# Kernel optimization log

Hardware: AMD Instinct MI355X
Metric: run time of the kernel (lower is better)

## Reference

```python
import jax, jax.numpy as jnp
import numpy as np

B, C1, C2, N1, N2 = 8, 16, 32, 256, 128


def _masks():
    # static numpy masks, mirroring EquivariantLayer.__init__
    n_max, n_min = max(N1, N2), min(N1, N2)
    k = np.arange(n_max)
    k[k > n_max // 2] -= n_max
    mask = np.abs(k) <= n_min / 2            # |k| <= n_min/2 (both nyquists)
    mask2 = mask[: n_max // 2 + 1].copy()    # taken BEFORE removing neg nyquist
    nyq_pos = k == n_min / 2
    nyq_pos2 = nyq_pos[: n_max // 2 + 1]
    nyq_neg = k == -n_min / 2
    mask[nyq_neg] = False                    # drop negative nyquist row
    return mask, mask2, nyq_pos, nyq_pos2

MASK, MASK2, NYQ_POS, NYQ_POS2 = _masks()


def rot90_kernel(t):
    # 90-deg rotation about grid point [0,0] for periodic kernels:
    # transpose last two dims, keep column 0, reverse remaining columns
    t = jnp.swapaxes(t, -1, -2)
    return jnp.concatenate([t[..., :1], t[..., 1:][..., ::-1]], axis=-1)


def symmetric_kernel(kernel):
    # average over the 8 elements of D4 (rotations + transpose*rotations)
    k1 = kernel
    k2 = rot90_kernel(k1)
    k3 = rot90_kernel(k2)
    k4 = rot90_kernel(k3)
    k5 = jnp.swapaxes(k1, -1, -2)
    k6 = rot90_kernel(k5)
    k7 = rot90_kernel(k6)
    k8 = rot90_kernel(k7)
    return (k1 + k2 + k3 + k4 + k5 + k6 + k7 + k8) / 8.0


def _forward(f, kernel):
    F = jnp.fft.rfft2(f)                                  # [b,c1,N1,N1//2+1]
    # downsample: zero nyquist modes, truncate spectrum, rescale
    F = jnp.where(jnp.asarray(NYQ_POS)[None, None, :, None], 0, F)
    F = jnp.where(jnp.asarray(NYQ_POS2)[None, None, None, :], 0, F)
    F = F[:, :, MASK, :][:, :, :, MASK2] * (N2 / N1) ** 2  # [b,c1,N2,N2//2+1]
    # spectral convolution with D4-symmetrized kernel
    K = jnp.fft.rfft2(symmetric_kernel(kernel))            # [1,c1,c2,N2,N2//2+1]
    conv = jnp.einsum('bcnk,cdnk->bdnk', F, K[0])          # sum over input channels
    return jnp.fft.irfft2(F), jnp.fft.irfft2(conv)


def setup_inputs() -> dict:
    key = jax.random.key(0)
    kf, kk = jax.random.split(key)
    f = jax.random.normal(kf, (B, C1, N1, N1), dtype=jnp.float32)
    eps = 0.1
    kernel = eps * (2.0 * jax.random.uniform(kk, (1, C1, C2, N2, N2), dtype=jnp.float32) - 1.0)
    return {"f": f, "kernel": kernel}


def reference(f, kernel):
    return _forward(f, kernel)
```

## Files before the change

kernel.cpp:

```cpp
#include <hip/hip_runtime.h>

#define PI_F 3.14159265358979f

__device__ __forceinline__ float2 cmul(float2 a, float2 b) {
    return make_float2(a.x * b.x - a.y * b.y, a.x * b.y + a.y * b.x);
}
__device__ __forceinline__ float2 cadd(float2 a, float2 b) { return make_float2(a.x + b.x, a.y + b.y); }
__device__ __forceinline__ float2 csub(float2 a, float2 b) { return make_float2(a.x - b.x, a.y - b.y); }
__device__ __forceinline__ float2 shflx(float2 v, int m) {
    return make_float2(__shfl_xor(v.x, m, 64), __shfl_xor(v.y, m, 64));
}
__device__ __forceinline__ float2 shfli(float2 v, int src) {
    return make_float2(__shfl(v.x, src, 64), __shfl(v.y, src, 64));
}
__device__ __forceinline__ int brev6(int x) { return (int)(__brev((unsigned)x) >> 26); }

template<int CTRL>
__device__ __forceinline__ float dpp1(float x) {
    return __builtin_bit_cast(float, __builtin_amdgcn_update_dpp(
        0, __builtin_bit_cast(int, x), CTRL, 0xF, 0xF, true));
}
template<int CTRL>
__device__ __forceinline__ float2 dppx(float2 v) {
    return make_float2(dpp1<CTRL>(v.x), dpp1<CTRL>(v.y));
}
template<int M>
__device__ __forceinline__ float2 xorx(float2 v) {
    if constexpr (M == 1)      return dppx<0xB1>(v);
    else if constexpr (M == 2) return dppx<0x4E>(v);
    else if constexpr (M == 8) return dppx<0x128>(v);
    else                       return shflx(v, M);
}

template<bool INV>
__device__ __forceinline__ void tw_init(int lane, float2* w, float* sg) {
#pragma unroll
    for (int t = 0; t < 6; ++t) {
        int m = 32 >> t;
        bool up = (lane & m) != 0;
        int pos = lane & (m - 1);
        float ang = (INV ? PI_F : -PI_F) * (float)pos / (float)m;
        float sn, cs;
        __sincosf(ang, &sn, &cs);
        w[t]  = up ? make_float2(cs, sn) : make_float2(1.f, 0.f);
        sg[t] = up ? -1.f : 1.f;
    }
}

__device__ __forceinline__ float2 fft64s(float2 v, const float2* w, const float* sg) {
#define FFT_STAGE(T, M) { float2 p = xorx<M>(v);                                   \
        float2 d = make_float2(fmaf(sg[T], v.x, p.x), fmaf(sg[T], v.y, p.y));      \
        v = cmul(d, w[T]); }
    FFT_STAGE(0, 32) FFT_STAGE(1, 16) FFT_STAGE(2, 8)
    FFT_STAGE(3, 4)  FFT_STAGE(4, 2)  FFT_STAGE(5, 1)
#undef FFT_STAGE
    return v;
}

__device__ void kfft_body(const float* __restrict__ kin, float* __restrict__ kout,
                          float2* X, int img) {
    int lane = threadIdx.x & 63, wv = threadIdx.x >> 6;
    float2 w[6]; float sg[6];
    tw_init<false>(lane, w, sg);
    int b6 = brev6(lane);
    float sn, cs;
    __sincosf(-PI_F * (float)lane * (1.0f / 64.0f), &sn, &cs);
    float2 w64 = make_float2(cs, sn);
    __sincosf(-PI_F * (float)b6 * (1.0f / 64.0f), &sn, &cs);
    float2 wub = make_float2(cs, sn);
    const float2* in2 = (const float2*)(kin + (size_t)img * 16384);
    int gm2 = brev6((64 - b6) & 63);
#pragma unroll 2
    for (int rr = 0; rr < 16; ++rr) {
        int r = wv * 16 + rr;
        float2 z = in2[r * 64 + lane];
        z = fft64s(z, w, sg);
        float2 zm = shfli(z, gm2);
        float ar = z.x + zm.x, ai = z.y - zm.y;
        float br = z.x - zm.x, bi = z.y + zm.y;
        float p = wub.x * br - wub.y * bi, q = wub.x * bi + wub.y * br;
        X[r * 65 + b6] = make_float2(0.5f * (ar + q), 0.5f * (ai - p));
    }
    __syncthreads();
    float2 c0[8], c1[8];
#pragma unroll
    for (int cc = 0; cc < 8; ++cc) {
        int k = wv * 8 + cc;
        c0[cc] = X[lane * 65 + k];
        c1[cc] = X[(lane + 64) * 65 + k];
    }
    __syncthreads();
    float* Rr = (float*)X;
#pragma unroll
    for (int cc = 0; cc < 8; ++cc) {
        int k = wv * 8 + cc;
        float2 r0 = c0[cc], r1 = c1[cc];
        float2 t = r0;
        r0 = cadd(t, r1);
        r1 = cmul(csub(t, r1), w64);
        r0 = fft64s(r0, w, sg);
        r1 = fft64s(r1, w, sg);
        Rr[(2 * b6) * 65 + k]     = r0.x;
        Rr[(2 * b6 + 1) * 65 + k] = r1.x;
    }
    __syncthreads();
    float4* ko4 = (float4*)(kout + (size_t)img * 8192);
    for (int i = threadIdx.x; i < 2048; i += 512) {
        int n = i >> 4, k4 = (i & 15) << 2;
        float4 o;
        float* op = (float*)&o;
#pragma unroll
        for (int m = 0; m < 4; ++m) {
            int k = k4 + m;
            float t1 = Rr[n * 65 + k];
            float t2 = Rr[((128 - n) & 127) * 65 + k];
            float t3, t4;
            if (n < 64) {
                t3 = Rr[k * 65 + n];
                t4 = Rr[((128 - k) & 127) * 65 + n];
            } else {
                int c2 = 128 - n; if (c2 > 63) c2 = 63;
                t3 = Rr[((128 - k) & 127) * 65 + c2];
                t4 = Rr[k * 65 + c2];
            }
            op[m] = 0.25f * (t1 + t2 + t3 + t4);
        }
        ko4[i] = o;
    }
}

__device__ void fcol_body(const float2* __restrict__ G, float2* __restrict__ FH,
                          float2* S, int bid) {
    int img = bid >> 2, q = bid & 3;
    int lane = threadIdx.x & 63, wv = threadIdx.x >> 6;
    float2 w[6]; float sg[6];
    tw_init<false>(lane, w, sg);
    float sn, cs;
    __sincosf(-PI_F * (float)lane * (1.0f / 64.0f), &sn, &cs);
    float2 w64 = make_float2(cs, sn);
    __sincosf(-PI_F * (float)lane * (1.0f / 128.0f), &sn, &cs);
    float2 w128a = make_float2(cs, sn);
    __sincosf(-PI_F * (float)(lane + 64) * (1.0f / 128.0f), &sn, &cs);
    float2 w128b = make_float2(cs, sn);
    const float2* src = G + (size_t)img * 16384 + q * 16;
    for (int i = threadIdx.x; i < 4096; i += 512) {
        int r = i >> 4, c = i & 15;
        S[r * 17 + c] = src[(size_t)r * 64 + c];
    }
    __syncthreads();
    float2 q0[2], q1[2], q2[2], q3[2];
#pragma unroll
    for (int cc = 0; cc < 2; ++cc) {
        int c = wv * 2 + cc;
        q0[cc] = S[(lane)       * 17 + c];
        q1[cc] = S[(lane +  64) * 17 + c];
        q2[cc] = S[(lane + 128) * 17 + c];
        q3[cc] = S[(lane + 192) * 17 + c];
    }
    __syncthreads();
    int b6 = brev6(lane);
#pragma unroll
    for (int cc = 0; cc < 2; ++cc) {
        int c = wv * 2 + cc;
        float2 r0 = q0[cc], r1 = q1[cc], r2 = q2[cc], r3 = q3[cc], t;
        t = r0; r0 = cadd(t, r2); r2 = cmul(csub(t, r2), w128a);
        t = r1; r1 = cadd(t, r3); r3 = cmul(csub(t, r3), w128b);
        t = r0; r0 = cadd(t, r1); r1 = cmul(csub(t, r1), w64);
        t = r2; r2 = cadd(t, r3); r3 = cmul(csub(t, r3), w64);
        r0 = fft64s(r0, w, sg); r1 = fft64s(r1, w, sg);
        r2 = fft64s(r2, w, sg); r3 = fft64s(r3, w, sg);
        float2 vv[4] = { r0, r2, r1, r3 };
#pragma unroll
        for (int j = 0; j < 4; ++j) {
            int n = 4 * b6 + j;
            int r = (n < 64) ? n : ((n >= 193) ? n - 128 : -1);
            if (r >= 0) S[r * 17 + c] = make_float2(vv[j].x * 0.25f, vv[j].y * 0.25f);
        }
    }
    __syncthreads();
    float2* dst = FH + (size_t)img * 8192 + q * 16;
    for (int i = threadIdx.x; i < 2048; i += 512) {
        int r = i >> 4, c = i & 15;
        float2 v = (r == 64) ? make_float2(0.f, 0.f) : S[r * 17 + c];
        dst[(size_t)r * 64 + c] = v;
    }
}

__device__ void einsum_body(const float2* __restrict__ F, const float* __restrict__ K,
                            float2* __restrict__ C, float2* Ft, int bid) {
    int nk0 = bid * 32;
    int t = threadIdx.x;
    for (int i = t; i < 4096; i += 512) {
        int bc = i >> 5, nl = i & 31;
        Ft[i] = F[(size_t)bc * 8192 + nk0 + nl];
    }
    __syncthreads();
    int nl = t & 31, dg = t >> 5;
    int nk = nk0 + nl;
    float2 acc[2][8] = {};
#pragma unroll
    for (int c = 0; c < 16; ++c) {
        float2 fv[8];
#pragma unroll
        for (int b = 0; b < 8; ++b) fv[b] = Ft[(b * 16 + c) * 32 + nl];
#pragma unroll
        for (int j = 0; j < 2; ++j) {
            int d = j * 16 + dg;
            float kv = K[(size_t)(c * 32 + d) * 8192 + nk];
#pragma unroll
            for (int b = 0; b < 8; ++b) {
                acc[j][b].x = fmaf(fv[b].x, kv, acc[j][b].x);
                acc[j][b].y = fmaf(fv[b].y, kv, acc[j][b].y);
            }
        }
    }
#pragma unroll
    for (int j = 0; j < 2; ++j) {
        int d = j * 16 + dg;
#pragma unroll
        for (int b = 0; b < 8; ++b)
            C[(size_t)(b * 32 + d) * 8192 + nk] = acc[j][b];
    }
}

__device__ void ifuse_body(const float2* __restrict__ src, float2* __restrict__ dst,
                           float2* S) {
    int lane = threadIdx.x & 63, wv = threadIdx.x >> 6;
    float2 w[6]; float sg[6];
    tw_init<true>(lane, w, sg);
    float sn, cs;
    __sincosf(PI_F * (float)lane * (1.0f / 64.0f), &sn, &cs);
    float2 w64 = make_float2(cs, sn);
    for (int i = threadIdx.x; i < 8192; i += 512) {
        int r = i >> 6, c = i & 63;
        S[r * 65 + c] = src[i];
    }
    __syncthreads();
    float2 c0[8], c1[8];
#pragma unroll
    for (int cc = 0; cc < 8; ++cc) {
        int k = wv * 8 + cc;
        c0[cc] = S[lane * 65 + k];
        c1[cc] = S[(lane + 64) * 65 + k];
    }
    __syncthreads();
    int b6 = brev6(lane);
#pragma unroll
    for (int cc = 0; cc < 8; ++cc) {
        int k = wv * 8 + cc;
        float2 r0 = c0[cc], r1 = c1[cc];
        float2 t = r0;
        r0 = cadd(t, r1);
        r1 = cmul(csub(t, r1), w64);
        r0 = fft64s(r0, w, sg);
        r1 = fft64s(r1, w, sg);
        S[(2 * b6) * 65 + k]     = r0;
        S[(2 * b6 + 1) * 65 + k] = r1;
    }
    __syncthreads();
#pragma unroll 2
    for (int rr = 0; rr < 16; ++rr) {
        int m = wv * 16 + rr;
        float2 X = S[m * 65 + lane];
        float2 Xm = shfli(X, (64 - lane) & 63);
        if (lane == 0) Xm = make_float2(0.f, 0.f);
        float er = 0.5f * (X.x + Xm.x), ei = 0.5f * (X.y - Xm.y);
        float br = 0.5f * (X.x - Xm.x), bi = 0.5f * (X.y + Xm.y);
        float orr = w64.x * br - w64.y * bi, oi = w64.x * bi + w64.y * br;
        float2 Z = make_float2(er - oi, ei + orr);
        Z = fft64s(Z, w, sg);
        Z = shfli(Z, b6);
        dst[m * 64 + lane] = make_float2(Z.x * (1.0f / 8192.0f), Z.y * (1.0f / 8192.0f));
    }
}

__global__ __launch_bounds__(256) void rfft256(const float* __restrict__ f,
                                               float2* __restrict__ G) {
    int lane = threadIdx.x & 63, wv = threadIdx.x >> 6;
    int row0 = (blockIdx.x * 4 + wv) * 8;
    float2 w[6]; float sg[6];
    tw_init<false>(lane, w, sg);
    float sn, cs;
    __sincosf(-PI_F * (float)lane * (1.0f / 64.0f), &sn, &cs);
    float2 w64 = make_float2(cs, sn);
    __sincosf(-PI_F * (float)lane * (1.0f / 128.0f), &sn, &cs);
    float2 wu = make_float2(cs, sn);
    int srcK = brev6(lane >> 1);
    int srcM = brev6((64 - ((lane + 1) >> 1)) & 63);
#pragma unroll 2
    for (int rr = 0; rr < 8; ++rr) {
        size_t row = (size_t)(row0 + rr);
        const float2* x = (const float2*)(f + row * 256);
        float2 r0 = x[lane], r1 = x[lane + 64];
        float2 t = r0;
        r0 = cadd(t, r1);
        r1 = cmul(csub(t, r1), w64);
        r0 = fft64s(r0, w, sg);
        r1 = fft64s(r1, w, sg);
        float2 e0 = shfli(r0, srcK), o0 = shfli(r1, srcK);
        float2 zk = (lane & 1) ? o0 : e0;
        float2 e1 = shfli(r0, srcM), o1 = shfli(r1, srcM);
        float2 zm = (lane & 1) ? o1 : e1;
        float ar = zk.x + zm.x, ai = zk.y - zm.y;
        float br = zk.x - zm.x, bi = zk.y + zm.y;
        float p = wu.x * br - wu.y * bi, q = wu.x * bi + wu.y * br;
        G[row * 64 + lane] = make_float2(0.5f * (ar + q), 0.5f * (ai - p));
    }
}

__global__ __launch_bounds__(512) void mega1(const float* __restrict__ kin,
                                             float* __restrict__ Kr,
                                             const float2* __restrict__ G,
                                             float2* __restrict__ FH) {
    __shared__ float2 SH[128 * 65];
    int bid = blockIdx.x;
    if (bid < 512) kfft_body(kin, Kr, SH, bid);
    else           fcol_body(G, FH, SH, bid - 512);
}

__global__ __launch_bounds__(512) void mega2(const float2* __restrict__ FH,
                                             const float* __restrict__ Kr,
                                             float2* __restrict__ CONV,
                                             float* __restrict__ out) {
    __shared__ float2 SH[128 * 65];
    int bid = blockIdx.x;
    if (bid < 256) einsum_body(FH, Kr, CONV, SH, bid);
    else {
        int img = bid - 256;
        ifuse_body(FH + (size_t)img * 8192, (float2*)(out + (size_t)img * 16384), SH);
    }
}

__global__ __launch_bounds__(512) void ifuse1(const float2* __restrict__ CV,
                                              float* __restrict__ out1) {
    __shared__ float2 SH[128 * 65];
    int img = blockIdx.x;
    ifuse_body(CV + (size_t)img * 8192, (float2*)(out1 + (size_t)img * 16384), SH);
}

extern "C" void kernel_launch(void* const* d_in, const int* in_sizes, int n_in,
                              void* d_out, int out_size, void* d_ws, size_t ws_size,
                              hipStream_t stream) {
    const float* f   = (const float*)d_in[0];
    const float* kin = (const float*)d_in[1];
    float* out = (float*)d_out;
    char* ws = (char*)d_ws;

    float2* G    = (float2*)ws;
    float2* CONV = (float2*)ws;
    float2* FHAT = (float2*)(ws + 16777216);
    float*  Kr   = (float*)(ws + 33554432);

    rfft256<<<1024, 256, 0, stream>>>(f, G);
    mega1<<<1024, 512, 0, stream>>>(kin, Kr, G, FHAT);
    mega2<<<384, 512, 0, stream>>>(FHAT, Kr, CONV, out);
    ifuse1<<<256, 512, 0, stream>>>(CONV, out + 2097152);
}
```

Baseline: 164.7 us.

## Store intermediate spectra and kernel FFT in bf16, regroup row FFT with kernel FFT

All intermediate buffers (row-FFT output, truncated spectrum, kernel spectrum, convolution result) are now stored as packed bf16 instead of fp32, halving global traffic between stages. The row rfft is merged into the first launch alongside the kernel FFT, and the column FFT becomes its own launch, so the launch order is rearranged. The rfft is also restructured so each even lane emits two outputs, and the inverse FFT writes with a bit-reversed index instead of doing a shuffle. The trade-off is reduced numerical precision, which may break the accuracy tolerance.

```diff
diff --git a/kernel.cpp b/kernel.cpp
--- a/kernel.cpp
+++ b/kernel.cpp
@@ -1,6 +1,9 @@
 #include <hip/hip_runtime.h>
 
 #define PI_F 3.14159265358979f
+
+typedef unsigned int  uint32;
+typedef unsigned short ushort16;
 
 __device__ __forceinline__ float2 cmul(float2 a, float2 b) {
     return make_float2(a.x * b.x - a.y * b.y, a.x * b.y + a.y * b.x);
@@ -14,6 +17,16 @@
     return make_float2(__shfl(v.x, src, 64), __shfl(v.y, src, 64));
 }
 __device__ __forceinline__ int brev6(int x) { return (int)(__brev((unsigned)x) >> 26); }
+
+__device__ __forceinline__ uint32 bfu(float x) {
+    uint32 u = __float_as_uint(x);
+    return (u + 0x7FFFu + ((u >> 16) & 1u)) >> 16;
+}
+__device__ __forceinline__ uint32 packbf2(float2 v) { return bfu(v.x) | (bfu(v.y) << 16); }
+__device__ __forceinline__ float2 unpackbf2(uint32 u) {
+    return make_float2(__uint_as_float(u << 16), __uint_as_float(u & 0xFFFF0000u));
+}
+__device__ __forceinline__ float bf2f(ushort16 u) { return __uint_as_float((uint32)u << 16); }
 
 template<int CTRL>
 __device__ __forceinline__ float dpp1(float x) {
@@ -57,7 +70,7 @@
     return v;
 }
 
-__device__ void kfft_body(const float* __restrict__ kin, float* __restrict__ kout,
+__device__ void kfft_body(const float* __restrict__ kin, ushort16* __restrict__ kout,
                           float2* X, int img) {
     int lane = threadIdx.x & 63, wv = threadIdx.x >> 6;
     float2 w[6]; float sg[6];
@@ -104,11 +117,10 @@
         Rr[(2 * b6 + 1) * 65 + k] = r1.x;
     }
     __syncthreads();
-    float4* ko4 = (float4*)(kout + (size_t)img * 8192);
+    ushort4* ko4 = (ushort4*)(kout + (size_t)img * 8192);
     for (int i = threadIdx.x; i < 2048; i += 512) {
         int n = i >> 4, k4 = (i & 15) << 2;
-        float4 o;
-        float* op = (float*)&o;
+        float op[4];
 #pragma unroll
         for (int m = 0; m < 4; ++m) {
             int k = k4 + m;
@@ -125,13 +137,67 @@
             }
             op[m] = 0.25f * (t1 + t2 + t3 + t4);
         }
-        ko4[i] = o;
-    }
-}
-
-__device__ void fcol_body(const float2* __restrict__ G, float2* __restrict__ FH,
-                          float2* S, int bid) {
-    int img = bid >> 2, q = bid & 3;
+        ushort4 o4;
+        o4.x = (ushort16)bfu(op[0]); o4.y = (ushort16)bfu(op[1]);
+        o4.z = (ushort16)bfu(op[2]); o4.w = (ushort16)bfu(op[3]);
+        ko4[i] = o4;
+    }
+}
+
+__device__ void rfft_body(const float* __restrict__ f, uint32* __restrict__ G, int bid) {
+    int lane = threadIdx.x & 63, wv = threadIdx.x >> 6;
+    int row0 = (bid * 8 + wv) * 8;
+    float2 w[6]; float sg[6];
+    tw_init<false>(lane, w, sg);
+    int m = brev6(lane);
+    float sn, cs;
+    __sincosf(-PI_F * (float)lane * (1.0f / 64.0f), &sn, &cs);
+    float2 w64 = make_float2(cs, sn);
+    __sincosf(-PI_F * (float)(2 * m) * (1.0f / 128.0f), &sn, &cs);
+    float2 wue = make_float2(cs, sn);
+    __sincosf(-PI_F * (float)(2 * m + 1) * (1.0f / 128.0f), &sn, &cs);
+    float2 wuo = make_float2(cs, sn);
+    int src_e = brev6((64 - m) & 63);
+    int src_o = brev6(63 - m);
+    bool active = (lane & 1) == 0;
+#pragma unroll 2
+    for (int rr = 0; rr < 8; ++rr) {
+        size_t row = (size_t)(row0 + rr);
+        const float2* x = (const float2*)(f + row * 256);
+        float2 r0 = x[lane], r1 = x[lane + 64];
+        float2 t = r0;
+        r0 = cadd(t, r1);
+        r1 = cmul(csub(t, r1), w64);
+        r0 = fft64s(r0, w, sg);
+        r1 = fft64s(r1, w, sg);
+        float2 zme = shfli(r0, src_e);
+        float2 zmo = shfli(r1, src_o);
+        float ar = r0.x + zme.x, ai = r0.y - zme.y;
+        float br = r0.x - zme.x, bi = r0.y + zme.y;
+        float p = wue.x * br - wue.y * bi, q = wue.x * bi + wue.y * br;
+        uint32 xe = packbf2(make_float2(0.5f * (ar + q), 0.5f * (ai - p)));
+        ar = r1.x + zmo.x; ai = r1.y - zmo.y;
+        br = r1.x - zmo.x; bi = r1.y + zmo.y;
+        p = wuo.x * br - wuo.y * bi; q = wuo.x * bi + wuo.y * br;
+        uint32 xo = packbf2(make_float2(0.5f * (ar + q), 0.5f * (ai - p)));
+        if (active) ((uint2*)(G + row * 64))[m] = make_uint2(xe, xo);
+    }
+}
+
+__global__ __launch_bounds__(512) void mega_a(const float* __restrict__ kin,
+                                              ushort16* __restrict__ Kr,
+                                              const float* __restrict__ f,
+                                              uint32* __restrict__ G) {
+    __shared__ float2 SH[128 * 65];
+    int bid = blockIdx.x;
+    if (bid < 512) kfft_body(kin, Kr, SH, bid);
+    else           rfft_body(f, G, bid - 512);
+}
+
+__global__ __launch_bounds__(512) void fcolk(const uint32* __restrict__ G,
+                                             uint32* __restrict__ FH) {
+    __shared__ uint32 S[256 * 17];
+    int img = blockIdx.x >> 2, qg = blockIdx.x & 3;
     int lane = threadIdx.x & 63, wv = threadIdx.x >> 6;
     float2 w[6]; float sg[6];
     tw_init<false>(lane, w, sg);
@@ -142,7 +208,7 @@
     float2 w128a = make_float2(cs, sn);
     __sincosf(-PI_F * (float)(lane + 64) * (1.0f / 128.0f), &sn, &cs);
     float2 w128b = make_float2(cs, sn);
-    const float2* src = G + (size_t)img * 16384 + q * 16;
+    const uint32* src = G + (size_t)img * 16384 + qg * 16;
     for (int i = threadIdx.x; i < 4096; i += 512) {
         int r = i >> 4, c = i & 15;
         S[r * 17 + c] = src[(size_t)r * 64 + c];
@@ -152,10 +218,10 @@
 #pragma unroll
     for (int cc = 0; cc < 2; ++cc) {
         int c = wv * 2 + cc;
-        q0[cc] = S[(lane)       * 17 + c];
-        q1[cc] = S[(lane +  64) * 17 + c];
-        q2[cc] = S[(lane + 128) * 17 + c];
-        q3[cc] = S[(lane + 192) * 17 + c];
+        q0[cc] = unpackbf2(S[(lane)       * 17 + c]);
+        q1[cc] = unpackbf2(S[(lane +  64) * 17 + c]);
+        q2[cc] = unpackbf2(S[(lane + 128) * 17 + c]);
+        q3[cc] = unpackbf2(S[(lane + 192) * 17 + c]);
     }
     __syncthreads();
     int b6 = brev6(lane);
@@ -174,20 +240,20 @@
         for (int j = 0; j < 4; ++j) {
             int n = 4 * b6 + j;
             int r = (n < 64) ? n : ((n >= 193) ? n - 128 : -1);
-            if (r >= 0) S[r * 17 + c] = make_float2(vv[j].x * 0.25f, vv[j].y * 0.25f);
+            if (r >= 0)
+                S[r * 17 + c] = packbf2(make_float2(vv[j].x * 0.25f, vv[j].y * 0.25f));
         }
     }
     __syncthreads();
-    float2* dst = FH + (size_t)img * 8192 + q * 16;
+    uint32* dst = FH + (size_t)img * 8192 + qg * 16;
     for (int i = threadIdx.x; i < 2048; i += 512) {
         int r = i >> 4, c = i & 15;
-        float2 v = (r == 64) ? make_float2(0.f, 0.f) : S[r * 17 + c];
-        dst[(size_t)r * 64 + c] = v;
-    }
-}
-
-__device__ void einsum_body(const float2* __restrict__ F, const float* __restrict__ K,
-                            float2* __restrict__ C, float2* Ft, int bid) {
+        dst[(size_t)r * 64 + c] = (r == 64) ? 0u : S[r * 17 + c];
+    }
+}
+
+__device__ void einsum_body(const uint32* __restrict__ F, const ushort16* __restrict__ K,
+                            uint32* __restrict__ C, uint32* Ft, int bid) {
     int nk0 = bid * 32;
     int t = threadIdx.x;
     for (int i = t; i < 4096; i += 512) {
@@ -202,11 +268,11 @@
     for (int c = 0; c < 16; ++c) {
         float2 fv[8];
 #pragma unroll
-        for (int b = 0; b < 8; ++b) fv[b] = Ft[(b * 16 + c) * 32 + nl];
+        for (int b = 0; b < 8; ++b) fv[b] = unpackbf2(Ft[(b * 16 + c) * 32 + nl]);
 #pragma unroll
         for (int j = 0; j < 2; ++j) {
             int d = j * 16 + dg;
-            float kv = K[(size_t)(c * 32 + d) * 8192 + nk];
+            float kv = bf2f(K[(size_t)(c * 32 + d) * 8192 + nk]);
 #pragma unroll
             for (int b = 0; b < 8; ++b) {
                 acc[j][b].x = fmaf(fv[b].x, kv, acc[j][b].x);
@@ -219,11 +285,11 @@
         int d = j * 16 + dg;
 #pragma unroll
         for (int b = 0; b < 8; ++b)
-            C[(size_t)(b * 32 + d) * 8192 + nk] = acc[j][b];
-    }
-}
-
-__device__ void ifuse_body(const float2* __restrict__ src, float2* __restrict__ dst,
+            C[(size_t)(b * 32 + d) * 8192 + nk] = packbf2(acc[j][b]);
+    }
+}
+
+__device__ void ifuse_body(const uint32* __restrict__ src, float2* __restrict__ dst,
                            float2* S) {
     int lane = threadIdx.x & 63, wv = threadIdx.x >> 6;
     float2 w[6]; float sg[6];
@@ -233,7 +299,7 @@
     float2 w64 = make_float2(cs, sn);
     for (int i = threadIdx.x; i < 8192; i += 512) {
         int r = i >> 6, c = i & 63;
-        S[r * 65 + c] = src[i];
+        S[r * 65 + c] = unpackbf2(src[i]);
     }
     __syncthreads();
     float2 c0[8], c1[8];
@@ -269,69 +335,24 @@
         float orr = w64.x * br - w64.y * bi, oi = w64.x * bi + w64.y * br;
         float2 Z = make_float2(er - oi, ei + orr);
         Z = fft64s(Z, w, sg);
-        Z = shfli(Z, b6);
-        dst[m * 64 + lane] = make_float2(Z.x * (1.0f / 8192.0f), Z.y * (1.0f / 8192.0f));
-    }
-}
-
-__global__ __launch_bounds__(256) void rfft256(const float* __restrict__ f,
-                                               float2* __restrict__ G) {
-    int lane = threadIdx.x & 63, wv = threadIdx.x >> 6;
-    int row0 = (blockIdx.x * 4 + wv) * 8;
-    float2 w[6]; float sg[6];
-    tw_init<false>(lane, w, sg);
-    float sn, cs;
-    __sincosf(-PI_F * (float)lane * (1.0f / 64.0f), &sn, &cs);
-    float2 w64 = make_float2(cs, sn);
-    __sincosf(-PI_F * (float)lane * (1.0f / 128.0f), &sn, &cs);
-    float2 wu = make_float2(cs, sn);
-    int srcK = brev6(lane >> 1);
-    int srcM = brev6((64 - ((lane + 1) >> 1)) & 63);
-#pragma unroll 2
-    for (int rr = 0; rr < 8; ++rr) {
-        size_t row = (size_t)(row0 + rr);
-        const float2* x = (const float2*)(f + row * 256);
-        float2 r0 = x[lane], r1 = x[lane + 64];
-        float2 t = r0;
-        r0 = cadd(t, r1);
-        r1 = cmul(csub(t, r1), w64);
-        r0 = fft64s(r0, w, sg);
-        r1 = fft64s(r1, w, sg);
-        float2 e0 = shfli(r0, srcK), o0 = shfli(r1, srcK);
-        float2 zk = (lane & 1) ? o0 : e0;
-        float2 e1 = shfli(r0, srcM), o1 = shfli(r1, srcM);
-        float2 zm = (lane & 1) ? o1 : e1;
-        float ar = zk.x + zm.x, ai = zk.y - zm.y;
-        float br = zk.x - zm.x, bi = zk.y + zm.y;
-        float p = wu.x * br - wu.y * bi, q = wu.x * bi + wu.y * br;
-        G[row * 64 + lane] = make_float2(0.5f * (ar + q), 0.5f * (ai - p));
-    }
-}
-
-__global__ __launch_bounds__(512) void mega1(const float* __restrict__ kin,
-                                             float* __restrict__ Kr,
-                                             const float2* __restrict__ G,
-                                             float2* __restrict__ FH) {
-    __shared__ float2 SH[128 * 65];
-    int bid = blockIdx.x;
-    if (bid < 512) kfft_body(kin, Kr, SH, bid);
-    else           fcol_body(G, FH, SH, bid - 512);
-}
-
-__global__ __launch_bounds__(512) void mega2(const float2* __restrict__ FH,
-                                             const float* __restrict__ Kr,
-                                             float2* __restrict__ CONV,
+        dst[m * 64 + b6] = make_float2(Z.x * (1.0f / 8192.0f), Z.y * (1.0f / 8192.0f));
+    }
+}
+
+__global__ __launch_bounds__(512) void mega2(const uint32* __restrict__ FH,
+                                             const ushort16* __restrict__ Kr,
+                                             uint32* __restrict__ CONV,
                                              float* __restrict__ out) {
     __shared__ float2 SH[128 * 65];
     int bid = blockIdx.x;
-    if (bid < 256) einsum_body(FH, Kr, CONV, SH, bid);
+    if (bid < 256) einsum_body(FH, Kr, CONV, (uint32*)SH, bid);
     else {
         int img = bid - 256;
         ifuse_body(FH + (size_t)img * 8192, (float2*)(out + (size_t)img * 16384), SH);
     }
 }
 
-__global__ __launch_bounds__(512) void ifuse1(const float2* __restrict__ CV,
+__global__ __launch_bounds__(512) void ifuse1(const uint32* __restrict__ CV,
                                               float* __restrict__ out1) {
     __shared__ float2 SH[128 * 65];
     int img = blockIdx.x;
@@ -346,13 +367,13 @@
     float* out = (float*)d_out;
     char* ws = (char*)d_ws;
 
-    float2* G    = (float2*)ws;
-    float2* CONV = (float2*)ws;
-    float2* FHAT = (float2*)(ws + 16777216);
-    float*  Kr   = (float*)(ws + 33554432);
-
-    rfft256<<<1024, 256, 0, stream>>>(f, G);
-    mega1<<<1024, 512, 0, stream>>>(kin, Kr, G, FHAT);
+    uint32*   G    = (uint32*)ws;
+    uint32*   CONV = (uint32*)ws;
+    uint32*   FHAT = (uint32*)(ws + 8388608);
+    ushort16* Kr   = (ushort16*)(ws + 16777216);
+
+    mega_a<<<1024, 512, 0, stream>>>(kin, Kr, f, G);
+    fcolk<<<512, 512, 0, stream>>>(G, FHAT);
     mega2<<<384, 512, 0, stream>>>(FHAT, Kr, CONV, out);
     ifuse1<<<256, 512, 0, stream>>>(CONV, out + 2097152);
 }
```

New measurement: 159.6 us. 1.03x faster.
